# Performance work log

Hardware: AMD Instinct MI355X
Metric: run time of the kernel (lower is better)

The kernel has to match this reference:

```python
import jax, jax.numpy as jnp
import numpy as np

B, SEQ, NV = 4, 1024, 32
PL, D, H, E_LAYERS, DFF = 16, 512, 8, 4, 2048
P = SEQ // PL  # 64 patches -> L = P*NV = 2048 tokens
WIN = 4
DH = D // H
SCALE = float(1.0 / np.sqrt(DH))


def layernorm(x, g, b):
    m = x.mean(-1, keepdims=True)
    v = jnp.var(x, axis=-1, keepdims=True)
    return (x - m) / jnp.sqrt(v + 1e-5) * g + b


def setup_inputs() -> dict:
    key = jax.random.key(0)
    ks = jax.random.split(key, 32)
    s = 0.02
    d = {}
    d['x_enc'] = jax.random.normal(ks[0], (B, SEQ, NV), jnp.float32)
    d['mask'] = jax.random.uniform(ks[1], (B, P, NV)) < 0.5  # mask_ratio=0.5
    d['W_embed'] = jax.random.normal(ks[2], (PL, D), jnp.float32) * s
    d['b_embed'] = jnp.zeros((D,), jnp.float32)
    per = lambda k, shp: jax.random.normal(k, (E_LAYERS,) + shp, jnp.float32) * s
    d['Wq'] = per(ks[3], (D, D)); d['bq'] = jnp.zeros((E_LAYERS, D))
    d['Wk'] = per(ks[4], (D, D)); d['bk'] = jnp.zeros((E_LAYERS, D))
    d['Wv'] = per(ks[5], (D, D)); d['bv'] = jnp.zeros((E_LAYERS, D))
    d['Wo'] = per(ks[6], (D, D)); d['bo'] = jnp.zeros((E_LAYERS, D))
    d['W1'] = per(ks[7], (D, DFF)); d['b1'] = jnp.zeros((E_LAYERS, DFF))
    d['W2'] = per(ks[8], (DFF, D)); d['b2'] = jnp.zeros((E_LAYERS, D))
    d['g1'] = jnp.ones((E_LAYERS, D)); d['be1'] = jnp.zeros((E_LAYERS, D))
    d['g2'] = jnp.ones((E_LAYERS, D)); d['be2'] = jnp.zeros((E_LAYERS, D))
    d['gf'] = jnp.ones((D,)); d['bf'] = jnp.zeros((D,))
    d['W_proj'] = jax.random.normal(ks[9], (D, PL), jnp.float32) * s
    d['b_proj'] = jnp.zeros((PL,), jnp.float32)
    return d


def reference(x_enc, mask, W_embed, b_embed, Wq, bq, Wk, bk, Wv, bv, Wo, bo,
              W1, b1, W2, b2, g1, be1, g2, be2, gf, bf, W_proj, b_proj):
    # instance norm over time (means detached, stdev differentiable as in torch)
    means = jax.lax.stop_gradient(x_enc.mean(1, keepdims=True))
    x = x_enc - means
    stdev = jnp.sqrt(jnp.var(x, axis=1, keepdims=True) + 1e-5)
    x = x / stdev
    # patchify: [B, P, NV, PL]
    patches = x[:, :P * PL, :].reshape(B, P, PL, NV).transpose(0, 1, 3, 2)
    emb = patches @ W_embed + b_embed                  # [B,P,NV,D]
    emb = jnp.where(mask[..., None], 0.0, emb)         # zero masked patches
    tok = emb.reshape(B, P * NV, D)                    # [B,L,D]
    # local/banded attention mask over patch index
    pid = jnp.arange(P * NV) // NV
    bad = jnp.abs(pid[:, None] - pid[None, :]) > WIN   # [L,L] True = masked
    for l in range(E_LAYERS):
        q = (tok @ Wq[l] + bq[l]).reshape(B, -1, H, DH)
        k = (tok @ Wk[l] + bk[l]).reshape(B, -1, H, DH)
        v = (tok @ Wv[l] + bv[l]).reshape(B, -1, H, DH)
        scores = jnp.einsum('blhe,bshe->bhls', q, k)
        scores = jnp.where(bad[None, None], -jnp.inf, scores)
        A = jax.nn.softmax(SCALE * scores, axis=-1)
        o = jnp.einsum('bhls,bshe->blhe', A, v).reshape(B, -1, D)
        tok = layernorm(tok + (o @ Wo[l] + bo[l]), g1[l], be1[l])
        y = jax.nn.gelu(tok @ W1[l] + b1[l], approximate=False) @ W2[l] + b2[l]
        tok = layernorm(tok + y, g2[l], be2[l])
    tok = layernorm(tok, gf, bf)
    enc = tok.reshape(B, P, NV, D)
    recon = enc @ W_proj + b_proj                      # [B,P,NV,PL]
    sc = stdev[:, 0, :][:, None, :, None]
    bi = means[:, 0, :][:, None, :, None]
    recon = recon * sc + bi
    target = patches * sc + bi
    mf = mask[..., None].astype(recon.dtype)
    denom = mf.sum() * PL
    denom = jnp.where(denom == 0, 1.0, denom)
    return (((recon - target) ** 2) * mf).sum() / denom
```

## Files before the change

kernel.cpp:

```cpp
#include <hip/hip_runtime.h>
#include <hip/hip_bf16.h>

#define DEV __device__ __forceinline__

namespace {

constexpr int Bn  = 4, SEQ = 1024, NV = 32, PL = 16, D = 512, H = 8, DFF = 2048;
constexpr int P   = SEQ / PL;
constexpr int L   = P * NV;
constexpr int M   = Bn * L;
constexpr int WIN = 4;

using short8   = __attribute__((ext_vector_type(8))) short;
using ushort8  = __attribute__((ext_vector_type(8))) unsigned short;
using float4v  = __attribute__((ext_vector_type(4))) float;

DEV float b2f(unsigned short u) { return __uint_as_float(((unsigned)u) << 16); }
DEV unsigned short f2b(float f) {
  unsigned fb = __float_as_uint(f);
  return (unsigned short)((fb + 0x7FFFu + ((fb >> 16) & 1u)) >> 16);
}
DEV unsigned short f2bt(float f) {
  return (unsigned short)(__float_as_uint(f) >> 16);
}
DEV float ldf(const void* p, size_t idx, int bf) {
  if (bf) return b2f(((const unsigned short*)p)[idx]);
  return ((const float*)p)[idx];
}
DEV void gll16(const void* gp, void* lp) {
  __builtin_amdgcn_global_load_lds(
      (const __attribute__((address_space(1))) void*)gp,
      (__attribute__((address_space(3))) void*)lp, 16, 0, 0);
}

__global__ void k_setup(const void* gf, const void* mask_raw, int* mask_i,
                        int* flags, float* scal) {
  __shared__ int s_gt1, s_oth, s_cnt;
  int tid = threadIdx.x;
  if (tid == 0) { s_gt1 = 0; s_oth = 0; s_cnt = 0; }
  __syncthreads();
  const unsigned* mw = (const unsigned*)mask_raw;
  int gt1 = 0, oth = 0;
  for (int i = tid; i < 2048; i += 256) {
    unsigned w = mw[i];
    if (w > 1u) { gt1 = 1; if (w != 0x3F800000u) oth = 1; }
  }
  if (gt1) atomicOr(&s_gt1, 1);
  if (oth) atomicOr(&s_oth, 1);
  __syncthreads();
  int fmt = (!s_gt1) ? 0 : (!s_oth ? 1 : 2);
  int cnt = 0;
  for (int i = tid; i < Bn * P * NV; i += 256) {
    int m;
    if (fmt == 0)      m = ((const int*)mask_raw)[i] != 0;
    else if (fmt == 1) m = ((const float*)mask_raw)[i] != 0.0f;
    else               m = ((const unsigned char*)mask_raw)[i] != 0;
    mask_i[i] = m; cnt += m;
  }
  atomicAdd(&s_cnt, cnt);
  __syncthreads();
  if (tid == 0) {
    unsigned w = *(const unsigned*)gf;
    flags[0] = ((w & 0xFFFFu) == 0x3F80u) ? 1 : 0;
    flags[1] = s_cnt;
    scal[0] = 0.f;
  }
}

__global__ void k_prep(const void* x, const void* bq, const void* bk,
                       const void* bv, const void* bo, const void* b1,
                       const void* b2, const void* gf, const void* bff,
                       const void* Wp, const void* bp, const int* flags,
                       float* means, float* stdev, float* biasf, float* lnw,
                       unsigned short* WpT) {
  int bf = flags[0];
  int tid = threadIdx.x;
  if (blockIdx.x < 32) {
    int bv_ = blockIdx.x * 4 + (tid >> 6);
    int b = bv_ >> 5, v = bv_ & 31;
    int lane = tid & 63;
    float s = 0.f, s2 = 0.f;
    for (int t = lane; t < SEQ; t += 64) {
      float val = ldf(x, (size_t)b * SEQ * NV + (size_t)t * NV + v, bf);
      s += val; s2 += val * val;
    }
    for (int off = 32; off; off >>= 1) {
      s += __shfl_xor(s, off); s2 += __shfl_xor(s2, off);
    }
    if (lane == 0) {
      float m = s / (float)SEQ;
      means[bv_] = m;
      stdev[bv_] = sqrtf(s2 / (float)SEQ - m * m + 1e-5f);
    }
    return;
  }
  int i = (blockIdx.x - 32) * 256 + tid;
  if (i < 18432) {
    int l = i / 4608, r = i % 4608;
    if (r < 1536) {
      float v = (r < 512) ? ldf(bq, l * 512 + r, bf)
              : (r < 1024) ? ldf(bk, l * 512 + r - 512, bf)
                           : ldf(bv, l * 512 + r - 1024, bf);
      biasf[l * 1536 + r] = v;
    } else if (r < 2048) {
      biasf[6144 + l * 512 + (r - 1536)] = ldf(bo, l * 512 + r - 1536, bf);
    } else if (r < 4096) {
      biasf[8192 + l * 2048 + (r - 2048)] = ldf(b1, l * 2048 + r - 2048, bf);
    } else {
      biasf[16384 + l * 512 + (r - 4096)] = ldf(b2, l * 512 + r - 4096, bf);
    }
  } else if (i < 19456) {
    int j = i - 18432;
    lnw[j] = (j < 512) ? ldf(gf, j, bf) : ldf(bff, j - 512, bf);
  } else if (i < 19472) {
    lnw[1024 + (i - 19456)] = ldf(bp, i - 19456, bf);
  } else if (i < 27664) {
    int j = i - 19472; int t = j >> 9, d = j & 511;
    WpT[j] = f2b(ldf(Wp, d * 16 + t, bf));
  }
}

__global__ void k_transpose_all(const void* Wq, const void* Wk, const void* Wv,
                                const void* Wo, const void* W1, const void* W2,
                                unsigned short* qkvT, unsigned short* WoT,
                                unsigned short* W1T, unsigned short* W2T,
                                const int* flags) {
  int bf = flags[0];
  int id = blockIdx.x;
  const void* src; unsigned short* dst;
  int Kd, Nd, l, n0, k0, dstOff = 0;
  size_t srcLS, dstLS;
  if (id < 4096) {
    int tensor = id >> 10, rem = id & 1023;
    l = rem >> 8; int t = rem & 255;
    n0 = (t & 15) * 32; k0 = (t >> 4) * 32;
    Kd = 512; Nd = 512; srcLS = 262144;
    if (tensor == 0)      { src = Wq; dst = qkvT; dstLS = 786432; dstOff = 0; }
    else if (tensor == 1) { src = Wk; dst = qkvT; dstLS = 786432; dstOff = 262144; }
    else if (tensor == 2) { src = Wv; dst = qkvT; dstLS = 786432; dstOff = 524288; }
    else                  { src = Wo; dst = WoT;  dstLS = 262144; }
  } else if (id < 8192) {
    int rem = id - 4096; l = rem >> 10; int t = rem & 1023;
    n0 = (t & 63) * 32; k0 = (t >> 6) * 32;
    Kd = 512; Nd = 2048; srcLS = 1048576; src = W1; dst = W1T; dstLS = 1048576;
  } else {
    int rem = id - 8192; l = rem >> 10; int t = rem & 1023;
    n0 = (t & 15) * 32; k0 = (t >> 4) * 32;
    Kd = 2048; Nd = 512; srcLS = 1048576; src = W2; dst = W2T; dstLS = 1048576;
  }
  int tx = threadIdx.x & 31, ty = threadIdx.x >> 5;
  __shared__ float tile[32][33];
  for (int rr = ty; rr < 32; rr += 8)
    tile[rr][tx] =
        ldf(src, (size_t)l * srcLS + (size_t)(k0 + rr) * Nd + n0 + tx, bf);
  __syncthreads();
  for (int rr = ty; rr < 32; rr += 8)
    dst[(size_t)l * dstLS + dstOff + (size_t)(n0 + rr) * Kd + k0 + tx] =
        f2b(tile[tx][rr]);
}

__global__ void k_embed(const void* x, const void* We, const void* be,
                        const int* flags, const int* mask_i,
                        const float* means, const float* stdev,
                        float* patches, unsigned short* tok) {
  int idx = blockIdx.x;
  int b = idx >> 11, pv = idx & 2047, p = pv >> 5, v = pv & 31;
  int bf = flags[0];
  __shared__ float pvs[PL];
  int tid = threadIdx.x;
  float m = means[b * NV + v], sd = stdev[b * NV + v];
  if (tid < PL) {
    float val =
        (ldf(x, (size_t)b * SEQ * NV + (size_t)(p * PL + tid) * NV + v, bf) -
         m) / sd;
    pvs[tid] = val;
    patches[(size_t)idx * PL + tid] = val;
  }
  __syncthreads();
  int masked = mask_i[idx];
  for (int d = tid; d < D; d += 128) {
    float acc = ldf(be, d, bf);
    for (int t = 0; t < PL; t++) acc += pvs[t] * ldf(We, t * D + d, bf);
    tok[(size_t)idx * D + d] = masked ? f2b(0.f) : f2b(acc);
  }
}

template <int BM, int BN, int WN>
__global__ __launch_bounds__(256) void k_gemm(
    const unsigned short* __restrict__ A, const unsigned short* __restrict__ W,
    const float* __restrict__ bias, const unsigned short* __restrict__ resid,
    unsigned short* __restrict__ C, unsigned short* __restrict__ vTp, int cs,
    int Kk, int act, int nbn) {
  constexpr int FI = 4, FJ = WN / 16, NWN = BN / WN;
  __shared__ __align__(16) char sm[BM * 128 + BN * 128];
  char* As = sm;
  char* Bs = sm + BM * 128;
  unsigned short* Cl = (unsigned short*)sm;
  int tid = threadIdx.x, lane = tid & 63, w = tid >> 6;
  int lane15 = lane & 15, q = lane >> 4;
  int wm = w / NWN, wn = w % NWN;
  int id = blockIdx.x;
  int xcd = id & 7, loc = id >> 3;
  int bn = (loc % nbn) * BN;
  int bm = (xcd * ((int)(gridDim.x >> 3) / nbn) + loc / nbn) * BM;
  int lrow = lane >> 3, lc = lane & 7;
  float4v acc[FI][FJ];
  for (int i = 0; i < FI; i++)
    for (int j = 0; j < FJ; j++) acc[i][j] = 0;
  for (int k0 = 0; k0 < Kk; k0 += 64) {
    if (k0) __syncthreads();
    for (int i = w; i < BM / 8; i += 4) {
      int row = i * 8 + lrow;
      gll16(A + (size_t)(bm + row) * Kk + k0 + ((lc ^ (row & 7)) << 3),
            As + i * 1024);
    }
    for (int i = w; i < BN / 8; i += 4) {
      int row = i * 8 + lrow;
      gll16(W + (size_t)(bn + row) * Kk + k0 + ((lc ^ (row & 7)) << 3),
            Bs + i * 1024);
    }
    __syncthreads();
    short8 a[2][FI], b[2][FJ];
    for (int h = 0; h < 2; h++) {
      for (int i = 0; i < FI; i++) {
        int rr = wm * 64 + i * 16 + lane15;
        a[h][i] =
            *(const short8*)(As + rr * 128 + (((h * 4 + q) ^ (rr & 7)) << 4));
      }
      for (int j = 0; j < FJ; j++) {
        int rr = wn * WN + j * 16 + lane15;
        b[h][j] =
            *(const short8*)(Bs + rr * 128 + (((h * 4 + q) ^ (rr & 7)) << 4));
      }
    }
    for (int h = 0; h < 2; h++)
      for (int i = 0; i < FI; i++)
        for (int j = 0; j < FJ; j++)
          acc[i][j] = __builtin_amdgcn_mfma_f32_16x16x32_bf16(
              a[h][i], b[h][j], acc[i][j], 0, 0, 0);
  }
  int vmode = (vTp != nullptr) && (bn >= 1024);
  float oscale = (vTp != nullptr && bn < 512) ? 0.125f : 1.0f;
  __syncthreads();
  for (int i = 0; i < FI; i++) {
    for (int j = 0; j < FJ; j++) {
      int col = wn * WN + j * 16 + lane15;
      float bv = bias[bn + col];
      for (int r = 0; r < 4; r++) {
        int row = wm * 64 + i * 16 + q * 4 + r;
        float cv = (acc[i][j][r] + bv) * oscale;
        if (act) {
          float t = cv * (1.5957692f + 0.0713548f * cv * cv);
          cv = cv / (1.f + __expf(-t));
        }
        if (!vmode)
          Cl[row * BN + (((col >> 3) ^ (row & 7)) << 3) + (col & 7)] = f2bt(cv);
        else
          Cl[col * BM + (((row >> 3) ^ (col & 7)) << 3) + (row & 7)] = f2bt(cv);
      }
    }
  }
  __syncthreads();
  if (!vmode) {
    constexpr int TOT = BM * BN / 8;
    for (int e = tid; e < TOT; e += 256) {
      int rr = e / (BN / 8), c8 = e % (BN / 8);
      ushort8 u = *(const ushort8*)(Cl + rr * BN + ((c8 ^ (rr & 7)) << 3));
      size_t off = (size_t)(bm + rr) * cs + bn + c8 * 8;
      if (resid) {
        ushort8 rv = *(const ushort8*)(resid + off);
        for (int t = 0; t < 8; t++) u[t] = f2bt(b2f(u[t]) + b2f(rv[t]));
      }
      *(ushort8*)(C + off) = u;
    }
  } else {
    constexpr int TOT = BM * BN / 8;
    for (int e = tid; e < TOT; e += 256) {
      int cc = e / (BM / 8), t8 = e % (BM / 8);
      ushort8 u = *(const ushort8*)(Cl + cc * BM + ((t8 ^ (cc & 7)) << 3));
      int hd = bn - 1024 + cc;
      int rowg = bm + t8 * 8;
      int bb = rowg >> 11, tokin = rowg & 2047;
      *(ushort8*)(vTp + ((size_t)(bb * 512 + hd)) * 2048 + tokin) = u;
    }
  }
}

__global__ __launch_bounds__(256) void k_attn(
    const unsigned short* __restrict__ qk,
    const unsigned short* __restrict__ vT, unsigned short* __restrict__ o) {
  constexpr int SSTR = 304;
  __shared__ __align__(16) unsigned short S[32 * SSTR];
  int id = blockIdx.x;
  int xcd = id & 7, rr_ = id >> 3;
  int p = xcd * 8 + (rr_ & 7);
  int h = (rr_ >> 3) & 7;
  int b = rr_ >> 6;
  int tid = threadIdx.x, lane = tid & 63, w = tid >> 6;
  int lane15 = lane & 15, q = lane >> 4;
  int p0 = max(0, p - WIN), p1 = min(P - 1, p + WIN);
  int nk = (p1 - p0 + 1) * 32;
  int ntiles = nk >> 4;
  size_t base = (size_t)b * L;
  short8 aq[2][2];
  for (int m = 0; m < 2; m++) {
    const unsigned short* qrow =
        qk + (base + p * 32 + m * 16 + lane15) * 1024 + h * 64 + q * 8;
    aq[m][0] = *(const short8*)(qrow);
    aq[m][1] = *(const short8*)(qrow + 32);
  }
  const unsigned short* kbase =
      qk + (base + p0 * 32) * 1024 + 512 + h * 64 + q * 8;
  {
    int nt = w;
    const unsigned short* kr = kbase + (size_t)(nt * 16 + lane15) * 1024;
    short8 c0, c1, n0, n1;
    if (nt < ntiles) {
      c0 = *(const short8*)(kr);
      c1 = *(const short8*)(kr + 32);
    }
    if (nt + 4 < ntiles) {
      kr = kbase + (size_t)((nt + 4) * 16 + lane15) * 1024;
      n0 = *(const short8*)(kr);
      n1 = *(const short8*)(kr + 32);
    }
    for (; nt < ntiles; nt += 4) {
      short8 m0, m1;
      if (nt + 8 < ntiles) {
        kr = kbase + (size_t)((nt + 8) * 16 + lane15) * 1024;
        m0 = *(const short8*)(kr);
        m1 = *(const short8*)(kr + 32);
      }
      for (int m = 0; m < 2; m++) {
        float4v s4 = 0;
        s4 = __builtin_amdgcn_mfma_f32_16x16x32_bf16(aq[m][0], c0, s4, 0, 0, 0);
        s4 = __builtin_amdgcn_mfma_f32_16x16x32_bf16(aq[m][1], c1, s4, 0, 0, 0);
        for (int r = 0; r < 4; r++)
          S[(m * 16 + q * 4 + r) * SSTR + nt * 16 + lane15] = f2b(s4[r]);
      }
      c0 = n0; c1 = n1; n0 = m0; n1 = m1;
    }
  }
  __syncthreads();
  {
    int row = tid >> 3, c = tid & 7;
    ushort8 eb[5];
    float sum = 0.f;
    for (int k = 0; k < 5; k++) {
      int j0 = c * 8 + k * 64;
      if (j0 < nk) {
        ushort8 u = *(const ushort8*)(S + row * SSTR + j0);
        ushort8 e8;
        for (int t = 0; t < 8; t++) {
          float e = __expf(b2f(u[t]));
          sum += e;
          e8[t] = f2bt(e);
        }
        eb[k] = e8;
      }
    }
    for (int off = 1; off < 8; off <<= 1) sum += __shfl_xor(sum, off);
    float inv = 1.f / sum;
    for (int k = 0; k < 5; k++) {
      int j0 = c * 8 + k * 64;
      if (j0 < nk) {
        ushort8 e8 = eb[k], u;
        for (int t = 0; t < 8; t++) u[t] = f2bt(b2f(e8[t]) * inv);
        *(ushort8*)(S + row * SSTR + j0) = u;
      }
    }
  }
  __syncthreads();
  int nkt = nk >> 5;
  const unsigned short* vb =
      vT + (size_t)(b * 512 + h * 64 + w * 16 + lane15) * 2048 + p0 * 32 +
      q * 8;
  const unsigned short* pr0 = S + lane15 * SSTR + q * 8;
  const unsigned short* pr1 = S + (16 + lane15) * SSTR + q * 8;
  float4v oa0 = 0, oa1 = 0;
  short8 ap0 = *(const short8*)(pr0);
  short8 ap1 = *(const short8*)(pr1);
  short8 v0 = *(const short8*)(vb);
  for (int kt = 0; kt < nkt; kt++) {
    short8 a0N, a1N, v0N;
    if (kt + 1 < nkt) {
      a0N = *(const short8*)(pr0 + (kt + 1) * 32);
      a1N = *(const short8*)(pr1 + (kt + 1) * 32);
      v0N = *(const short8*)(vb + (kt + 1) * 32);
    }
    oa0 = __builtin_amdgcn_mfma_f32_16x16x32_bf16(ap0, v0, oa0, 0, 0, 0);
    oa1 = __builtin_amdgcn_mfma_f32_16x16x32_bf16(ap1, v0, oa1, 0, 0, 0);
    ap0 = a0N; ap1 = a1N; v0 = v0N;
  }
  __syncthreads();
  for (int r = 0; r < 4; r++) {
    S[(q * 4 + r) * 72 + w * 16 + lane15] = f2bt(oa0[r]);
    S[(16 + q * 4 + r) * 72 + w * 16 + lane15] = f2bt(oa1[r]);
  }
  __syncthreads();
  {
    int row = tid >> 3, c8 = tid & 7;
    ushort8 val = *(const ushort8*)(S + row * 72 + c8 * 8);
    *(ushort8*)(o + (base + p * 32 + row) * 512 + h * 64 + c8 * 8) = val;
  }
}

__global__ void k_ln(const unsigned short* __restrict__ x, const void* g,
                     const void* bta, unsigned short* __restrict__ out,
                     const int* flags, int goff) {
  int bf = flags[0];
  int row = blockIdx.x * 4 + (threadIdx.x >> 6);
  int lane = threadIdx.x & 63;
  ushort8 u = *(const ushort8*)(x + (size_t)row * D + lane * 8);
  float v[8]; float s = 0.f, s2 = 0.f;
  for (int t = 0; t < 8; t++) {
    v[t] = b2f(u[t]); s += v[t]; s2 += v[t] * v[t];
  }
  for (int off = 32; off; off >>= 1) {
    s += __shfl_xor(s, off); s2 += __shfl_xor(s2, off);
  }
  float m = s / (float)D;
  float inv = rsqrtf(s2 / (float)D - m * m + 1e-5f);
  ushort8 ou;
  for (int t = 0; t < 8; t++) {
    int c = lane * 8 + t;
    ou[t] = f2b((v[t] - m) * inv * ldf(g, goff + c, bf) + ldf(bta, goff + c, bf));
  }
  *(ushort8*)(out + (size_t)row * D + lane * 8) = ou;
}

__global__ __launch_bounds__(128) void k_lnloss(
    const unsigned short* __restrict__ tok, const float* __restrict__ lnw,
    const unsigned short* __restrict__ WpT, const float* __restrict__ patches,
    const float* __restrict__ stdev, const int* __restrict__ mask_i,
    float* scal) {
  constexpr int RS = 520;
  __shared__ __align__(16) unsigned short As[32 * RS];
  __shared__ __align__(16) unsigned short Bs[16 * RS];
  int bpI = blockIdx.x; int b = bpI >> 6, p = bpI & 63;
  int tid = threadIdx.x;
  int row = tid >> 2, cg = tid & 3;
  size_t tokbase = (size_t)(b * L + p * 32);
  float s = 0.f, s2 = 0.f;
  for (int i = 0; i < 16; i++) {
    int c = cg + i * 4;
    ushort8 u = *(const ushort8*)(tok + (tokbase + row) * D + c * 8);
    for (int t = 0; t < 8; t++) { float v = b2f(u[t]); s += v; s2 += v * v; }
  }
  s += __shfl_xor(s, 1); s += __shfl_xor(s, 2);
  s2 += __shfl_xor(s2, 1); s2 += __shfl_xor(s2, 2);
  float m = s / (float)D;
  float inv = rsqrtf(s2 / (float)D - m * m + 1e-5f);
  for (int i = 0; i < 16; i++) {
    int c = cg + i * 4;
    ushort8 u = *(const ushort8*)(tok + (tokbase + row) * D + c * 8);
    ushort8 o;
    for (int t = 0; t < 8; t++) {
      int col = c * 8 + t;
      o[t] = f2b((b2f(u[t]) - m) * inv * lnw[col] + lnw[512 + col]);
    }
    *(ushort8*)(As + row * RS + c * 8) = o;
  }
  for (int e = tid; e < 16 * 64; e += 128) {
    int r = e >> 6, c = e & 63;
    *(ushort8*)(Bs + r * RS + c * 8) = *(const ushort8*)(WpT + r * 512 + c * 8);
  }
  __syncthreads();
  int w = tid >> 6, lane = tid & 63, lane15 = lane & 15, q = lane >> 4;
  float4v acc = 0;
  for (int kt = 0; kt < 16; kt++) {
    short8 a = *(const short8*)(As + (w * 16 + lane15) * RS + kt * 32 + q * 8);
    short8 bfr = *(const short8*)(Bs + lane15 * RS + kt * 32 + q * 8);
    acc = __builtin_amdgcn_mfma_f32_16x16x32_bf16(a, bfr, acc, 0, 0, 0);
  }
  float local = 0.f;
  int t = lane15;
  for (int r = 0; r < 4; r++) {
    int v = w * 16 + q * 4 + r;
    int tokidx = b * 2048 + p * 32 + v;
    if (mask_i[tokidx]) {
      float recon = acc[r] + lnw[1024 + t];
      float diff = recon - patches[(size_t)tokidx * 16 + t];
      float sc = stdev[b * 32 + v];
      local += sc * sc * diff * diff;
    }
  }
  for (int off = 32; off; off >>= 1) local += __shfl_xor(local, off);
  if (lane == 0) atomicAdd(&scal[0], local);
}

__global__ void k_final(const float* scal, const int* flags, unsigned* out) {
  float denom = (float)flags[1] * (float)PL;
  if (denom == 0.f) denom = 1.f;
  float loss = scal[0] / denom;
  unsigned fb = __float_as_uint(loss);
  unsigned u = (fb + 0x7FFFu + ((fb >> 16) & 1u)) >> 16;
  out[0] = (u << 16) | u;
}

}

extern "C" void kernel_launch(void* const* d_in, const int* in_sizes, int n_in,
                              void* d_out, int out_size, void* d_ws,
                              size_t ws_size, hipStream_t stream) {
  const void* x_enc = d_in[0];
  const void* maskp = d_in[1];
  const void* We = d_in[2];  const void* be_ = d_in[3];
  const void* Wq = d_in[4];  const void* bq = d_in[5];
  const void* Wk = d_in[6];  const void* bk = d_in[7];
  const void* Wv = d_in[8];  const void* bv = d_in[9];
  const void* Wo = d_in[10]; const void* bo_ = d_in[11];
  const void* W1 = d_in[12]; const void* b1 = d_in[13];
  const void* W2 = d_in[14]; const void* b2 = d_in[15];
  const void* g1 = d_in[16]; const void* be1 = d_in[17];
  const void* g2 = d_in[18]; const void* be2 = d_in[19];
  const void* gf = d_in[20]; const void* bff = d_in[21];
  const void* Wp = d_in[22]; const void* bp = d_in[23];

  constexpr size_t MB = 1u << 20;
  char* w = (char*)d_ws;
  int*   mask_i  = (int*)w;
  int*   flags   = (int*)(w + 32768);
  float* scal    = (float*)(w + 32896);
  float* means   = (float*)(w + 33024);
  float* stdev   = (float*)(w + 33600);
  float* biasf   = (float*)(w + 36864);
  float* lnw     = (float*)(w + 114688);
  float* patches = (float*)(w + 131072);
  unsigned short* WpT = (unsigned short*)(w + 655360);
  unsigned short* qkvT = (unsigned short*)(w + 1 * MB);
  unsigned short* WoT  = (unsigned short*)(w + 7 * MB);
  unsigned short* W1T  = (unsigned short*)(w + 9 * MB);
  unsigned short* W2T  = (unsigned short*)(w + 17 * MB);
  unsigned short* tok  = (unsigned short*)(w + 25 * MB);
  unsigned short* tmp  = (unsigned short*)(w + 33 * MB);
  unsigned short* ob   = (unsigned short*)(w + 41 * MB);
  unsigned short* qk   = (unsigned short*)(w + 49 * MB);
  unsigned short* vTb  = (unsigned short*)(w + 73 * MB);
  unsigned short* hidden = ob;

  k_setup<<<1, 256, 0, stream>>>(gf, maskp, mask_i, flags, scal);
  k_prep<<<141, 256, 0, stream>>>(x_enc, bq, bk, bv, bo_, b1, b2, gf, bff, Wp,
                                  bp, flags, means, stdev, biasf, lnw, WpT);
  k_transpose_all<<<12288, 256, 0, stream>>>(Wq, Wk, Wv, Wo, W1, W2, qkvT, WoT,
                                             W1T, W2T, flags);
  k_embed<<<M, 128, 0, stream>>>(x_enc, We, be_, flags, mask_i, means, stdev,
                                 patches, tok);
  for (int l = 0; l < 4; l++) {
    k_gemm<128, 64, 32><<<1536, 256, 0, stream>>>(
        tok, qkvT + (size_t)l * 786432, biasf + l * 1536, nullptr, qk, vTb,
        1024, 512, 0, 24);
    k_attn<<<2048, 256, 0, stream>>>(qk, vTb, ob);
    k_gemm<64, 64, 16><<<1024, 256, 0, stream>>>(
        ob, WoT + (size_t)l * 262144, biasf + 6144 + l * 512, tok, tmp,
        nullptr, 512, 512, 0, 8);
    k_ln<<<M / 4, 256, 0, stream>>>(tmp, g1, be1, tok, flags, l * 512);
    k_gemm<128, 64, 32><<<2048, 256, 0, stream>>>(
        tok, W1T + (size_t)l * 1048576, biasf + 8192 + l * 2048, nullptr,
        hidden, nullptr, 2048, 512, 1, 32);
    k_gemm<64, 64, 16><<<1024, 256, 0, stream>>>(
        hidden, W2T + (size_t)l * 1048576, biasf + 16384 + l * 512, tok, tmp,
        nullptr, 512, 2048, 0, 8);
    k_ln<<<M / 4, 256, 0, stream>>>(tmp, g2, be2, tok, flags, l * 512);
  }
  k_lnloss<<<Bn * P, 128, 0, stream>>>(tok, lnw, WpT, patches, stdev, mask_i,
                                       scal);
  k_final<<<1, 1, 0, stream>>>(scal, flags, (unsigned*)d_out);
}
```

Measured before the change: 875.7 us.

## Add 256x256-tile 8-wave GEMM with quadrant ping-pong for QKV and FFN1

Introduces a new GEMM kernel using 256x256 output tiles, 512 threads, and double-buffered LDS (128 KB). The kernel computes the tile in four quadrants, interleaving async global-to-LDS loads with MFMA phases under explicit barriers and priority hints. The QKV projection and the first FFN GEMM are switched to it, so each input byte is reused more from LDS and more MFMA work is done per byte. In exchange, the grid shrinks to 192/256 blocks with one block per CU, which risks underfilling the 256 CUs (notably for QKV) and losing latency hiding.

```diff
diff --git a/kernel.cpp b/kernel.cpp
--- a/kernel.cpp
+++ b/kernel.cpp
@@ -286,6 +286,194 @@
   }
 }
 
+#define G256_MM(QM, QN)                                                     \
+  {                                                                         \
+    __builtin_amdgcn_s_setprio(1);                                          \
+    _Pragma("unroll") for (int kh = 0; kh < 2; ++kh) {                      \
+      _Pragma("unroll") for (int mi = 0; mi < 2; ++mi) {                    \
+        _Pragma("unroll") for (int ni = 0; ni < 4; ++ni) {                  \
+          acc[QM][QN][mi][ni] = __builtin_amdgcn_mfma_f32_16x16x32_bf16(    \
+              a[mi][kh], b[ni][kh], acc[QM][QN][mi][ni], 0, 0, 0);          \
+        }                                                                   \
+      }                                                                     \
+    }                                                                       \
+    __builtin_amdgcn_s_setprio(0);                                          \
+  }
+
+DEV short8 g256_frag(const char* base, int R, int kh, int q) {
+  return *(const short8*)(base + R * 128 + (((kh * 4 + q) ^ (R & 7)) << 4));
+}
+
+DEV void g256_stage(const unsigned short* __restrict__ G, int row0, int Kk,
+                    int tt, char* region, int Hh, int w, int lrow, int lc) {
+#pragma unroll
+  for (int j = 0; j < 2; ++j) {
+    int R = Hh * 128 + j * 64 + w * 8 + lrow;
+    gll16(G + (size_t)(row0 + R) * Kk + tt * 64 + ((lc ^ (R & 7)) << 3),
+          region + (Hh * 128 + j * 64 + w * 8) * 128);
+  }
+}
+
+__global__ __launch_bounds__(512) void k_gemm256(
+    const unsigned short* __restrict__ A, const unsigned short* __restrict__ W,
+    const float* __restrict__ bias, const unsigned short* __restrict__ resid,
+    unsigned short* __restrict__ C, unsigned short* __restrict__ vTp, int cs,
+    int Kk, int act, int nbn) {
+  __shared__ __align__(16) char sm[131072];
+  unsigned short* Cl = (unsigned short*)sm;
+  int tid = threadIdx.x, lane = tid & 63, w = tid >> 6;
+  int lane15 = lane & 15, q = lane >> 4;
+  int lrow = lane >> 3, lc = lane & 7;
+  int wr = (w & 3) * 32;
+  int wc = (w >> 2) * 64;
+  int id = blockIdx.x;
+  int xcd = id & 7, loc = id >> 3;
+  int bn = (loc % nbn) * 256;
+  int bm = (xcd * ((int)(gridDim.x >> 3) / nbn) + loc / nbn) * 256;
+  int NT = Kk >> 6;
+
+  float4v acc[2][2][2][4];
+#pragma unroll
+  for (int i = 0; i < 2; i++)
+#pragma unroll
+    for (int j = 0; j < 2; j++)
+#pragma unroll
+      for (int mi = 0; mi < 2; mi++)
+#pragma unroll
+        for (int ni = 0; ni < 4; ni++) acc[i][j][mi][ni] = 0;
+
+  {
+    char* A0b = sm;
+    char* B0b = sm + 32768;
+    char* A1b = sm + 65536;
+    char* B1b = sm + 98304;
+    g256_stage(A, bm, Kk, 0, A0b, 0, w, lrow, lc);
+    g256_stage(A, bm, Kk, 0, A0b, 1, w, lrow, lc);
+    g256_stage(W, bn, Kk, 0, B0b, 0, w, lrow, lc);
+    g256_stage(W, bn, Kk, 0, B0b, 1, w, lrow, lc);
+    if (NT > 1) {
+      g256_stage(A, bm, Kk, 1, A1b, 0, w, lrow, lc);
+      g256_stage(W, bn, Kk, 1, B1b, 1, w, lrow, lc);
+      g256_stage(A, bm, Kk, 1, A1b, 1, w, lrow, lc);
+      asm volatile("s_waitcnt vmcnt(6)" ::: "memory");
+    } else {
+      asm volatile("s_waitcnt vmcnt(0)" ::: "memory");
+    }
+    __builtin_amdgcn_sched_barrier(0);
+    __builtin_amdgcn_s_barrier();
+  }
+
+  for (int t = 0; t < NT; ++t) {
+    char* Ac = sm + (t & 1) * 65536;
+    char* Bc = Ac + 32768;
+    char* An = sm + ((t + 1) & 1) * 65536;
+    char* Bnx = An + 32768;
+    short8 a[2][2], b[4][2];
+#pragma unroll
+    for (int mi = 0; mi < 2; ++mi)
+#pragma unroll
+      for (int kh = 0; kh < 2; ++kh)
+        a[mi][kh] = g256_frag(Ac, wr + mi * 16 + lane15, kh, q);
+#pragma unroll
+    for (int ni = 0; ni < 4; ++ni)
+#pragma unroll
+      for (int kh = 0; kh < 2; ++kh)
+        b[ni][kh] = g256_frag(Bc, wc + ni * 16 + lane15, kh, q);
+    if (t + 1 < NT) g256_stage(W, bn, Kk, t + 1, Bnx, 0, w, lrow, lc);
+    __builtin_amdgcn_s_barrier();
+    G256_MM(0, 0);
+    __builtin_amdgcn_s_barrier();
+#pragma unroll
+    for (int ni = 0; ni < 4; ++ni)
+#pragma unroll
+      for (int kh = 0; kh < 2; ++kh)
+        b[ni][kh] = g256_frag(Bc, 128 + wc + ni * 16 + lane15, kh, q);
+    if (t + 2 < NT) g256_stage(A, bm, Kk, t + 2, Ac, 0, w, lrow, lc);
+    __builtin_amdgcn_s_barrier();
+    G256_MM(0, 1);
+    __builtin_amdgcn_s_barrier();
+#pragma unroll
+    for (int mi = 0; mi < 2; ++mi)
+#pragma unroll
+      for (int kh = 0; kh < 2; ++kh)
+        a[mi][kh] = g256_frag(Ac, 128 + wr + mi * 16 + lane15, kh, q);
+    if (t + 2 < NT) g256_stage(W, bn, Kk, t + 2, Bc, 1, w, lrow, lc);
+    __builtin_amdgcn_s_barrier();
+    G256_MM(1, 1);
+    __builtin_amdgcn_s_barrier();
+#pragma unroll
+    for (int ni = 0; ni < 4; ++ni)
+#pragma unroll
+      for (int kh = 0; kh < 2; ++kh)
+        b[ni][kh] = g256_frag(Bc, wc + ni * 16 + lane15, kh, q);
+    if (t + 2 < NT) g256_stage(A, bm, Kk, t + 2, Ac, 1, w, lrow, lc);
+    if (t + 2 < NT) {
+      asm volatile("s_waitcnt vmcnt(6)" ::: "memory");
+    } else if (t + 1 < NT) {
+      asm volatile("s_waitcnt vmcnt(0)" ::: "memory");
+    }
+    __builtin_amdgcn_sched_barrier(0);
+    __builtin_amdgcn_s_barrier();
+    G256_MM(1, 0);
+    __builtin_amdgcn_s_barrier();
+  }
+
+  int vmode = (vTp != nullptr) && (bn >= 1024);
+  float oscale = (vTp != nullptr && bn < 512) ? 0.125f : 1.0f;
+  __syncthreads();
+#pragma unroll
+  for (int QM = 0; QM < 2; QM++) {
+#pragma unroll
+    for (int QN = 0; QN < 2; QN++) {
+#pragma unroll
+      for (int mi = 0; mi < 2; mi++) {
+#pragma unroll
+        for (int ni = 0; ni < 4; ni++) {
+          int col = QN * 128 + wc + ni * 16 + lane15;
+          float bv = bias[bn + col];
+#pragma unroll
+          for (int r = 0; r < 4; r++) {
+            int row = QM * 128 + wr + mi * 16 + q * 4 + r;
+            float cv = (acc[QM][QN][mi][ni][r] + bv) * oscale;
+            if (act) {
+              float tt = cv * (1.5957692f + 0.0713548f * cv * cv);
+              cv = cv / (1.f + __expf(-tt));
+            }
+            if (!vmode)
+              Cl[row * 256 + (((col >> 3) ^ (row & 7)) << 3) + (col & 7)] =
+                  f2bt(cv);
+            else
+              Cl[col * 256 + (((row >> 3) ^ (col & 7)) << 3) + (row & 7)] =
+                  f2bt(cv);
+          }
+        }
+      }
+    }
+  }
+  __syncthreads();
+  if (!vmode) {
+    for (int e = tid; e < 8192; e += 512) {
+      int rr = e >> 5, c8 = e & 31;
+      ushort8 u = *(const ushort8*)(Cl + rr * 256 + ((c8 ^ (rr & 7)) << 3));
+      size_t off = (size_t)(bm + rr) * cs + bn + c8 * 8;
+      if (resid) {
+        ushort8 rv = *(const ushort8*)(resid + off);
+        for (int t = 0; t < 8; t++) u[t] = f2bt(b2f(u[t]) + b2f(rv[t]));
+      }
+      *(ushort8*)(C + off) = u;
+    }
+  } else {
+    for (int e = tid; e < 8192; e += 512) {
+      int cc = e >> 5, t8 = e & 31;
+      ushort8 u = *(const ushort8*)(Cl + cc * 256 + ((t8 ^ (cc & 7)) << 3));
+      int hd = bn - 1024 + cc;
+      int rowg = bm + t8 * 8;
+      int bb = rowg >> 11, tokin = rowg & 2047;
+      *(ushort8*)(vTp + ((size_t)(bb * 512 + hd)) * 2048 + tokin) = u;
+    }
+  }
+}
+
 __global__ __launch_bounds__(256) void k_attn(
     const unsigned short* __restrict__ qk,
     const unsigned short* __restrict__ vT, unsigned short* __restrict__ o) {
@@ -547,17 +735,17 @@
   k_embed<<<M, 128, 0, stream>>>(x_enc, We, be_, flags, mask_i, means, stdev,
                                  patches, tok);
   for (int l = 0; l < 4; l++) {
-    k_gemm<128, 64, 32><<<1536, 256, 0, stream>>>(
+    k_gemm256<<<192, 512, 0, stream>>>(
         tok, qkvT + (size_t)l * 786432, biasf + l * 1536, nullptr, qk, vTb,
-        1024, 512, 0, 24);
+        1024, 512, 0, 6);
     k_attn<<<2048, 256, 0, stream>>>(qk, vTb, ob);
     k_gemm<64, 64, 16><<<1024, 256, 0, stream>>>(
         ob, WoT + (size_t)l * 262144, biasf + 6144 + l * 512, tok, tmp,
         nullptr, 512, 512, 0, 8);
     k_ln<<<M / 4, 256, 0, stream>>>(tmp, g1, be1, tok, flags, l * 512);
-    k_gemm<128, 64, 32><<<2048, 256, 0, stream>>>(
+    k_gemm256<<<256, 512, 0, stream>>>(
         tok, W1T + (size_t)l * 1048576, biasf + 8192 + l * 2048, nullptr,
-        hidden, nullptr, 2048, 512, 1, 32);
+        hidden, nullptr, 2048, 512, 1, 8);
     k_gemm<64, 64, 16><<<1024, 256, 0, stream>>>(
         hidden, W2T + (size_t)l * 1048576, biasf + 16384 + l * 512, tok, tmp,
         nullptr, 512, 2048, 0, 8);
```

New measurement: 892.7 us. Within noise of the previous version (+1.9%).
